# Kernel optimization log

Hardware: AMD Instinct MI355X
Metric: run time of the kernel (lower is better)

## Reference

```python
import jax, jax.numpy as jnp
import numpy as np

NUME = 100000
H, DH, K, R = 4, 32, 16, 17
DIN, DT, DOUT = 128, 32, 128
N0, N1, N2 = 131072, 32768, 4096
B, HIST = 2048, 2
LN_EPS = 1e-5


def setup_inputs() -> dict:
    key = jax.random.key(0)
    ks = jax.random.split(key, 16)
    din = DIN + DT
    inp = {}
    inp["emb"] = jax.random.normal(ks[0], (NUME, DIN), jnp.float32) * 0.1
    inp["freq"] = jnp.asarray(1.0 / 10 ** np.linspace(0, 9, DT), jnp.float32)
    inp["phase"] = jnp.zeros((DT,), jnp.float32)
    for l in (0, 1):
        inp[f"gamma{l}"] = jnp.ones((din,), jnp.float32)
        inp[f"beta{l}"] = jnp.zeros((din,), jnp.float32)
        inp[f"W{l}"] = jax.random.normal(ks[1 + 5 * l], (R, din, H * DH), jnp.float32) * 0.05
        inp[f"attn_l{l}"] = jax.random.normal(ks[2 + 5 * l], (R, H, DH), jnp.float32) * 0.05
        inp[f"attn_r{l}"] = jax.random.normal(ks[3 + 5 * l], (R, H, DH), jnp.float32) * 0.05
        inp[f"bias{l}"] = jnp.zeros((R, H * DH), jnp.float32)
    inp["src_ids0"] = jax.random.randint(ks[11], (N0,), 0, NUME * 100)
    inp["src_idx0"] = jax.random.randint(ks[12], (R, N1, K), 0, N0)
    inp["src_ids1"] = jax.random.randint(ks[13], (N1,), 0, NUME * 100)
    inp["src_idx1"] = jax.random.randint(ks[14], (R, N2, K), 0, N1)
    inp["root_idx"] = jax.random.randint(ks[15], (B * HIST,), 0, N2)
    inp["ts"] = 99
    return inp


def _gat_layer(h, src_ids, src_idx, gamma, beta, W, al, ar, b, ts, freq, phase):
    # h: [Nsrc, din-DT] src-node features; src_idx: [R, Ndst, K] neighbor ids.
    ndst = src_idx.shape[1]
    # TimeEnc: cos((ts - nid // nume) * freq + phase)
    t = (ts - src_ids // NUME).astype(h.dtype)
    phi = jnp.cos(t[:, None] * freq + phase)  # [Nsrc, DT]
    h = jnp.concatenate([h, phi], axis=1)
    # LayerNorm
    mu = jnp.mean(h, axis=-1, keepdims=True)
    var = jnp.mean((h - mu) ** 2, axis=-1, keepdims=True)
    h = (h - mu) * jax.lax.rsqrt(var + LN_EPS) * gamma + beta

    def body(acc, xs):
        Wr, alr, arr, br, idx = xs
        proj = (h @ Wr).reshape(-1, H, DH)               # [Nsrc, H, DH]
        el = jnp.einsum('nhe,he->nh', proj, alr)         # [Nsrc, H]
        er = jnp.einsum('nhe,he->nh', proj[:ndst], arr)  # [Ndst, H]
        e = jax.nn.leaky_relu(el[idx] + er[:, None, :], 0.2)  # [Ndst, K, H]
        a = jax.nn.softmax(e, axis=1)                    # edge softmax over K
        out = jnp.einsum('ikh,ikhe->ihe', a, proj[idx]) + br.reshape(H, DH)
        return acc + out, None

    acc, _ = jax.lax.scan(body, jnp.zeros((ndst, H, DH), h.dtype),
                          (W, al, ar, b, src_idx))
    # HeteroGraphConv aggregate='mean' over R relation outputs, then ReLU
    return jax.nn.relu((acc / R).reshape(ndst, H * DH))


def reference(emb, freq, phase,
              gamma0, beta0, W0, attn_l0, attn_r0, bias0,
              gamma1, beta1, W1, attn_l1, attn_r1, bias1,
              src_ids0, src_idx0, src_ids1, src_idx1, root_idx, ts):
    h = emb[src_ids0 % NUME]  # entity embedding lookup [N0, DIN]
    h = _gat_layer(h, src_ids0, src_idx0, gamma0, beta0, W0, attn_l0, attn_r0,
                   bias0, ts, freq, phase)
    h = _gat_layer(h, src_ids1, src_idx1, gamma1, beta1, W1, attn_l1, attn_r1,
                   bias1, ts, freq, phase)
    # gather root embeddings and fold hist dimension into features
    return h[root_idx].reshape(B, HIST * DOUT)
```

## Files before the change

kernel.cpp:

```cpp
#include <hip/hip_runtime.h>
#include <hip/hip_bf16.h>

#define NUME 100000
constexpr int H      = 4;
constexpr int DH     = 32;
constexpr int KNB    = 16;
constexpr int R      = 17;
constexpr int DIN    = 128;
constexpr int DT     = 32;
constexpr int DINT   = 160;
constexpr int N0     = 131072;
constexpr int N1     = 32768;
constexpr int N2     = 4096;
constexpr float LN_EPS = 1e-5f;

typedef unsigned short ushort_t;
typedef ushort_t us4 __attribute__((ext_vector_type(4)));
typedef ushort_t us8 __attribute__((ext_vector_type(8)));
typedef short    s8v __attribute__((ext_vector_type(8)));
typedef float    f32x4 __attribute__((ext_vector_type(4)));

__device__ __forceinline__ float bf2f(ushort_t u) {
    return __uint_as_float(((unsigned int)u) << 16);
}
__device__ __forceinline__ ushort_t f2bf(float f) {
    unsigned int x = __float_as_uint(f);
    unsigned int r = x + 0x7fffu + ((x >> 16) & 1u);
    return (ushort_t)(r >> 16);
}

__global__ __launch_bounds__(256) void k_wcast(
    const float* __restrict__ W, ushort_t* __restrict__ wt, int total)
{
    int t = blockIdx.x * blockDim.x + threadIdx.x;
    if (t >= total) return;
    int r   = t / (DINT * DIN);
    int rem = t % (DINT * DIN);
    int k   = rem >> 7;
    int n   = rem & 127;
    wt[(size_t)r * DIN * DINT + (size_t)n * DINT + k] = f2bf(W[t]);
}

__global__ __launch_bounds__(256) void k_bsum(
    const float* __restrict__ b0, const float* __restrict__ b1,
    float* __restrict__ bsum01)
{
    int t = threadIdx.x;
    const float* b = (t < 128) ? b0 : b1;
    int c = t & 127;
    float s = 0.f;
    #pragma unroll
    for (int r = 0; r < R; ++r) s += b[r * 128 + c];
    bsum01[t] = s;
}

__global__ __launch_bounds__(256) void k_prep(
    const float* __restrict__ srcf,
    const int*   __restrict__ ids,
    const int*   __restrict__ ts_ptr,
    const float* __restrict__ freq,
    const float* __restrict__ phase,
    const float* __restrict__ gamma,
    const float* __restrict__ beta,
    const float* __restrict__ bsum,
    ushort_t*    __restrict__ hn,
    int n_rows, int mode)
{
    int wv   = (int)((blockIdx.x * blockDim.x + threadIdx.x) >> 6);
    int lane = threadIdx.x & 63;
    int half = lane >> 5;
    int l5   = lane & 31;
    int row  = wv * 2 + half;
    if (row >= n_rows) return;

    int id = ids[row];
    const float* rp = (mode == 1)
        ? (srcf + (size_t)(id % NUME) * DIN)
        : (srcf + (size_t)row * DIN);

    float4 x = *(const float4*)&rp[l5 * 4];
    if (mode == 0) {
        const float4 bs = *(const float4*)&bsum[l5 * 4];
        x.x = fmaxf((x.x + bs.x) * (1.f / (float)R), 0.f);
        x.y = fmaxf((x.y + bs.y) * (1.f / (float)R), 0.f);
        x.z = fmaxf((x.z + bs.z) * (1.f / (float)R), 0.f);
        x.w = fmaxf((x.w + bs.w) * (1.f / (float)R), 0.f);
    }

    int   ts = ts_ptr[0];
    float t  = (float)(ts - id / NUME);
    float p  = cosf(t * freq[l5] + phase[l5]);

    float s  = x.x + x.y + x.z + x.w + p;
    float sq = x.x*x.x + x.y*x.y + x.z*x.z + x.w*x.w + p*p;
    #pragma unroll
    for (int m = 1; m < 32; m <<= 1) {
        s  += __shfl_xor(s,  m);
        sq += __shfl_xor(sq, m);
    }
    float mu   = s / (float)DINT;
    float var  = sq / (float)DINT - mu * mu;
    float rstd = rsqrtf(var + LN_EPS);

    size_t base = (size_t)row * DINT;
    us4 pk;
    pk[0] = f2bf((x.x - mu) * rstd * gamma[l5*4+0] + beta[l5*4+0]);
    pk[1] = f2bf((x.y - mu) * rstd * gamma[l5*4+1] + beta[l5*4+1]);
    pk[2] = f2bf((x.z - mu) * rstd * gamma[l5*4+2] + beta[l5*4+2]);
    pk[3] = f2bf((x.w - mu) * rstd * gamma[l5*4+3] + beta[l5*4+3]);
    *(us4*)&hn[base + l5*4] = pk;
    hn[base + 128 + l5] = f2bf((p - mu) * rstd * gamma[128 + l5] + beta[128 + l5]);
}

__global__ __launch_bounds__(256) void k_gemm(
    const ushort_t* __restrict__ A,
    const ushort_t* __restrict__ BtB,
    const float*    __restrict__ alB,
    const float*    __restrict__ arB,
    ushort_t*       __restrict__ CB,
    float*          __restrict__ elB,
    float*          __restrict__ erB,
    int ndst, int M)
{
    __shared__ ushort_t Bs[128][168];
    __shared__ ushort_t As[2][128][40];

    int r = blockIdx.y;
    const ushort_t* Bt = BtB + (size_t)r * DIN * DINT;
    const float*    al = alB + (size_t)r * DIN;
    const float*    ar = arB + (size_t)r * DIN;
    ushort_t*       C  = CB  + (size_t)r * M * DIN;
    float*          el = elB + (size_t)r * M * 4;
    float*          er = erB + (size_t)r * ndst * 4;

    int tid  = threadIdx.x;
    int lane = tid & 63;
    int wave = tid >> 6;
    int wr   = wave >> 1;
    int wc   = wave & 1;
    int row0 = blockIdx.x * 128;

    {
        int bm  = tid >> 1;
        int bko = (tid & 1) * 80;
        #pragma unroll
        for (int g = 0; g < 10; ++g)
            *(us8*)&Bs[bm][bko + g * 8] =
                *(const us8*)&Bt[(size_t)bm * DINT + bko + g * 8];
        #pragma unroll
        for (int j = 0; j < 2; ++j) {
            int f  = tid + j * 256;
            int m  = f >> 2;
            int ko = (f & 3) * 8;
            *(us8*)&As[0][m][ko] = *(const us8*)&A[(size_t)(row0 + m) * DINT + ko];
        }
    }
    __syncthreads();

    s8v breg[5][4];
    #pragma unroll
    for (int kk = 0; kk < 5; ++kk)
        #pragma unroll
        for (int j = 0; j < 4; ++j)
            breg[kk][j] = *(const s8v*)&Bs[wc*64 + j*16 + (lane & 15)]
                                          [kk*32 + (lane >> 4) * 8];

    f32x4 acc[4][4];
    #pragma unroll
    for (int i = 0; i < 4; ++i)
        #pragma unroll
        for (int j = 0; j < 4; ++j) acc[i][j] = (f32x4){0.f, 0.f, 0.f, 0.f};

    #pragma unroll
    for (int kc = 0; kc < 5; ++kc) {
        us8 pa[2];
        int m0 = 0, ko0 = 0, m1 = 0, ko1 = 0;
        if (kc < 4) {
            int f0 = tid;
            m0  = f0 >> 2; ko0 = (f0 & 3) * 8;
            pa[0] = *(const us8*)&A[(size_t)(row0 + m0) * DINT + (kc + 1) * 32 + ko0];
            int f1 = tid + 256;
            m1  = f1 >> 2; ko1 = (f1 & 3) * 8;
            pa[1] = *(const us8*)&A[(size_t)(row0 + m1) * DINT + (kc + 1) * 32 + ko1];
        }

        s8v af[4];
        #pragma unroll
        for (int i = 0; i < 4; ++i)
            af[i] = *(const s8v*)&As[kc & 1][wr*64 + i*16 + (lane & 15)]
                                            [(lane >> 4) * 8];
        #pragma unroll
        for (int i = 0; i < 4; ++i)
            #pragma unroll
            for (int j = 0; j < 4; ++j)
                acc[i][j] = __builtin_amdgcn_mfma_f32_16x16x32_bf16(
                                af[i], breg[kc][j], acc[i][j], 0, 0, 0);

        if (kc < 4) {
            *(us8*)&As[(kc + 1) & 1][m0][ko0] = pa[0];
            *(us8*)&As[(kc + 1) & 1][m1][ko1] = pa[1];
        }
        __syncthreads();
    }

    #pragma unroll
    for (int i = 0; i < 4; ++i) {
        #pragma unroll
        for (int j = 0; j < 4; ++j) {
            int col  = wc*64 + j*16 + (lane & 15);
            int rowb = row0 + wr*64 + i*16 + ((lane >> 4) << 2);
            #pragma unroll
            for (int q = 0; q < 4; ++q)
                C[(size_t)(rowb + q) * DIN + col] = f2bf(acc[i][j][q]);
        }
    }

    float alv[4], arv[4];
    #pragma unroll
    for (int j = 0; j < 4; ++j) {
        int c = wc*64 + j*16 + (lane & 15);
        alv[j] = al[c];
        arv[j] = ar[c];
    }
    int b0 = lane & 1;
    int b1 = (lane >> 1) & 1;
    #pragma unroll
    for (int i = 0; i < 4; ++i) {
        #pragma unroll
        for (int q = 0; q < 4; ++q) {
            float pl0 = acc[i][0][q]*alv[0] + acc[i][1][q]*alv[1];
            float pl1 = acc[i][2][q]*alv[2] + acc[i][3][q]*alv[3];
            float pr0 = acc[i][0][q]*arv[0] + acc[i][1][q]*arv[1];
            float pr1 = acc[i][2][q]*arv[2] + acc[i][3][q]*arv[3];
            float t;
            t = __shfl_xor(b0 ? pl0 : pl1, 1);
            float vA = (b0 ? pl1 : pl0) + t;
            t = __shfl_xor(b0 ? pr0 : pr1, 1);
            float vB = (b0 ? pr1 : pr0) + t;
            t = __shfl_xor(b1 ? vA : vB, 2);
            float vC = (b1 ? vB : vA) + t;
            vC += __shfl_xor(vC, 4);
            vC += __shfl_xor(vC, 8);
            if ((lane & 12) == 0) {
                int row = row0 + wr*64 + i*16 + ((lane >> 4) << 2) + q;
                int h   = 2*wc + b0;
                if (!b1) {
                    el[(size_t)row * 4 + h] = vC;
                } else if (row < ndst) {
                    er[(size_t)row * 4 + h] = vC;
                }
            }
        }
    }
}

__global__ __launch_bounds__(256) void k_agg_r(
    const ushort_t* __restrict__ proj,
    const int*      __restrict__ idx,
    const float*    __restrict__ el,
    const float*    __restrict__ er,
    float*          __restrict__ accg,
    int ndst)
{
    int wid  = (int)((blockIdx.x * blockDim.x + threadIdx.x) >> 6);
    if (wid >= ndst) return;
    int l    = threadIdx.x & 63;
    int rsub = l >> 4;
    int fg   = l & 15;

    int jv = idx[(size_t)wid * KNB + (l & 15)];

    int j2[4];
    us8 v[4];
    #pragma unroll
    for (int kk = 0; kk < 4; ++kk) j2[kk] = __shfl(jv, 4*kk + rsub);
    #pragma unroll
    for (int kk = 0; kk < 4; ++kk)
        v[kk] = *(const us8*)&proj[(size_t)j2[kk] * DIN + fg * 8];

    int   jk = __shfl(jv, l >> 2);
    float e  = el[(size_t)jk * 4 + (l & 3)] + er[(size_t)wid * 4 + (l & 3)];
    e = e > 0.f ? e : 0.2f * e;
    float mx = e;
    #pragma unroll
    for (int m = 4; m < 64; m <<= 1) mx = fmaxf(mx, __shfl_xor(mx, m));
    float p = __expf(e - mx);
    float s = p;
    #pragma unroll
    for (int m = 4; m < 64; m <<= 1) s += __shfl_xor(s, m);
    float a = p / s;

    float vacc[8];
    #pragma unroll
    for (int t = 0; t < 8; ++t) vacc[t] = 0.f;
    #pragma unroll
    for (int kk = 0; kk < 4; ++kk) {
        float ak = __shfl(a, 16*kk + 4*rsub + (fg >> 2));
        #pragma unroll
        for (int t = 0; t < 8; ++t) vacc[t] = fmaf(ak, bf2f(v[kk][t]), vacc[t]);
    }
    #pragma unroll
    for (int t = 0; t < 8; ++t) {
        vacc[t] += __shfl_xor(vacc[t], 16);
        vacc[t] += __shfl_xor(vacc[t], 32);
    }
    if (l < 16) {
        float* ap = accg + (size_t)wid * DIN + l * 8;
        #pragma unroll
        for (int t = 0; t < 8; ++t) ap[t] += vacc[t];
    }
}

__global__ __launch_bounds__(256) void k_agg_all(
    const ushort_t* __restrict__ projB,
    const int*      __restrict__ idxB,
    const float*    __restrict__ elB,
    const float*    __restrict__ erB,
    float*          __restrict__ accg,
    int ndst, int nsrc)
{
    int wid  = (int)((blockIdx.x * blockDim.x + threadIdx.x) >> 6);
    if (wid >= ndst) return;
    int l    = threadIdx.x & 63;
    int rsub = l >> 4;
    int fg   = l & 15;

    float vacc[8];
    #pragma unroll
    for (int t = 0; t < 8; ++t) vacc[t] = 0.f;

    for (int r = 0; r < R; ++r) {
        const ushort_t* proj = projB + (size_t)r * nsrc * DIN;
        const int*      idx  = idxB  + (size_t)r * ndst * KNB;
        const float*    el   = elB   + (size_t)r * nsrc * 4;
        const float*    er   = erB   + (size_t)r * ndst * 4;

        int jv = idx[(size_t)wid * KNB + (l & 15)];

        int j2[4];
        us8 v[4];
        #pragma unroll
        for (int kk = 0; kk < 4; ++kk) j2[kk] = __shfl(jv, 4*kk + rsub);
        #pragma unroll
        for (int kk = 0; kk < 4; ++kk)
            v[kk] = *(const us8*)&proj[(size_t)j2[kk] * DIN + fg * 8];

        int   jk = __shfl(jv, l >> 2);
        float e  = el[(size_t)jk * 4 + (l & 3)] + er[(size_t)wid * 4 + (l & 3)];
        e = e > 0.f ? e : 0.2f * e;
        float mx = e;
        #pragma unroll
        for (int m = 4; m < 64; m <<= 1) mx = fmaxf(mx, __shfl_xor(mx, m));
        float p = __expf(e - mx);
        float s = p;
        #pragma unroll
        for (int m = 4; m < 64; m <<= 1) s += __shfl_xor(s, m);
        float a = p / s;

        #pragma unroll
        for (int kk = 0; kk < 4; ++kk) {
            float ak = __shfl(a, 16*kk + 4*rsub + (fg >> 2));
            #pragma unroll
            for (int t = 0; t < 8; ++t) vacc[t] = fmaf(ak, bf2f(v[kk][t]), vacc[t]);
        }
    }

    #pragma unroll
    for (int t = 0; t < 8; ++t) {
        vacc[t] += __shfl_xor(vacc[t], 16);
        vacc[t] += __shfl_xor(vacc[t], 32);
    }
    if (l < 16) {
        float* ap = accg + (size_t)wid * DIN + l * 8;
        #pragma unroll
        for (int t = 0; t < 8; ++t) ap[t] = vacc[t];
    }
}

__global__ __launch_bounds__(256) void k_root(
    const float* __restrict__ acc, const int* __restrict__ root,
    const float* __restrict__ bsum1, float* __restrict__ out, int n)
{
    int t = blockIdx.x * blockDim.x + threadIdx.x;
    if (t < n) {
        float x = acc[(size_t)root[t >> 7] * DIN + (t & 127)] + bsum1[t & 127];
        out[t] = fmaxf(x * (1.f / (float)R), 0.f);
    }
}

extern "C" void kernel_launch(void* const* d_in, const int* in_sizes, int n_in,
                              void* d_out, int out_size, void* d_ws, size_t ws_size,
                              hipStream_t stream)
{
    const float* emb    = (const float*)d_in[0];
    const float* freq   = (const float*)d_in[1];
    const float* phase  = (const float*)d_in[2];
    const float* gamma0 = (const float*)d_in[3];
    const float* beta0  = (const float*)d_in[4];
    const float* W0     = (const float*)d_in[5];
    const float* al0    = (const float*)d_in[6];
    const float* ar0    = (const float*)d_in[7];
    const float* b0     = (const float*)d_in[8];
    const float* gamma1 = (const float*)d_in[9];
    const float* beta1  = (const float*)d_in[10];
    const float* W1     = (const float*)d_in[11];
    const float* al1    = (const float*)d_in[12];
    const float* ar1    = (const float*)d_in[13];
    const float* b1     = (const float*)d_in[14];
    const int* src_ids0 = (const int*)d_in[15];
    const int* src_idx0 = (const int*)d_in[16];
    const int* src_ids1 = (const int*)d_in[17];
    const int* src_idx1 = (const int*)d_in[18];
    const int* root     = (const int*)d_in[19];
    const int* ts       = (const int*)d_in[20];
    float* out = (float*)d_out;

    char* cur = (char*)d_ws;
    auto carve = [&](size_t bytes) {
        char* p = cur;
        cur += (bytes + 255) & ~(size_t)255;
        return (void*)p;
    };
    ushort_t* hn    = (ushort_t*)carve((size_t)N0 * DINT * 2);
    float*    acc   = (float*)carve((size_t)N1 * DIN * 4);
    ushort_t* wt0   = (ushort_t*)carve((size_t)R * DIN * DINT * 2);
    ushort_t* wt1   = (ushort_t*)carve((size_t)R * DIN * DINT * 2);
    float*    bsum  = (float*)carve(256 * 4);
    ushort_t* proj  = (ushort_t*)carve((size_t)N0 * DIN * 2);
    float*    el0   = (float*)carve((size_t)N0 * 4 * 4);
    float*    er0   = (float*)carve((size_t)N1 * 4 * 4);
    size_t baseC = (size_t)(cur - (char*)d_ws);
    ushort_t* proj1 = (ushort_t*)carve((size_t)R * N1 * DIN * 2);
    float*    el1   = (float*)carve((size_t)R * N1 * 4 * 4);
    float*    er1   = (float*)carve((size_t)R * N2 * 4 * 4);
    size_t needB = (size_t)(cur - (char*)d_ws);
    const bool batchedL1 = (ws_size >= needB);
    (void)baseC;

    const int WTOT = R * DINT * DIN;

    k_bsum<<<1, 256, 0, stream>>>(b0, b1, bsum);
    k_wcast<<<(WTOT + 255) / 256, 256, 0, stream>>>(W0, wt0, WTOT);
    k_wcast<<<(WTOT + 255) / 256, 256, 0, stream>>>(W1, wt1, WTOT);

    hipMemsetAsync(acc, 0, (size_t)N1 * DIN * sizeof(float), stream);
    k_prep<<<N0 / 8, 256, 0, stream>>>(emb, src_ids0, ts, freq, phase,
                                       gamma0, beta0, bsum, hn, N0, 1);
    for (int r = 0; r < R; ++r) {
        k_gemm<<<dim3(N0 / 128, 1), 256, 0, stream>>>(
            hn, wt0 + (size_t)r * DIN * DINT, al0 + r * 128, ar0 + r * 128,
            proj, el0, er0, N1, N0);
        k_agg_r<<<N1 / 4, 256, 0, stream>>>(
            proj, src_idx0 + (size_t)r * N1 * KNB, el0, er0, acc, N1);
    }

    k_prep<<<N1 / 8, 256, 0, stream>>>(acc, src_ids1, ts, freq, phase,
                                       gamma1, beta1, bsum, hn, N1, 0);
    if (batchedL1) {
        k_gemm<<<dim3(N1 / 128, R), 256, 0, stream>>>(
            hn, wt1, al1, ar1, proj1, el1, er1, N2, N1);
        k_agg_all<<<N2 / 4, 256, 0, stream>>>(
            proj1, src_idx1, el1, er1, acc, N2, N1);
    } else {
        hipMemsetAsync(acc, 0, (size_t)N2 * DIN * sizeof(float), stream);
        for (int r = 0; r < R; ++r) {
            k_gemm<<<dim3(N1 / 128, 1), 256, 0, stream>>>(
                hn, wt1 + (size_t)r * DIN * DINT, al1 + r * 128, ar1 + r * 128,
                proj, el0, er0, N2, N1);
            k_agg_r<<<N2 / 4, 256, 0, stream>>>(
                proj, src_idx1 + (size_t)r * N2 * KNB, el0, er0, acc, N2);
        }
    }

    k_root<<<(N2 * DIN) / 256, 256, 0, stream>>>(acc, root, bsum + 128, out, N2 * DIN);
}
```

Measured before the change: 1.208 ms.

## Batch GAT relations in groups of four and pad LDS tiles

Relations are now processed in groups of up to four. Each group gets one batched GEMM launch and one aggregation launch that sums the group's relations in registers before a single read-modify-write of the accumulator. The first group writes the accumulator directly, so the memset is no longer needed. This cuts per-relation launches and global accumulator traffic in layer 0, and replaces the fully batched layer-1 path with the same grouped scheme to bound workspace size. The GEMM shared-memory tiles also get an odd padding (170 and 42 elements) with split 8-byte LDS accesses to reduce bank conflicts, at the cost of more LDS instructions and 8-byte accesses that may not be 8-byte aligned.

```diff
diff --git a/kernel.cpp b/kernel.cpp
--- a/kernel.cpp
+++ b/kernel.cpp
@@ -28,6 +28,18 @@
     unsigned int r = x + 0x7fffu + ((x >> 16) & 1u);
     return (ushort_t)(r >> 16);
 }
+__device__ __forceinline__ void st_us8_2(ushort_t* p, us8 v) {
+    *(us4*)p       = __builtin_shufflevector(v, v, 0, 1, 2, 3);
+    *(us4*)(p + 4) = __builtin_shufflevector(v, v, 4, 5, 6, 7);
+}
+__device__ __forceinline__ s8v ld_s8v_2(const ushort_t* p) {
+    us4 a = *(const us4*)p;
+    us4 b = *(const us4*)(p + 4);
+    us8 t = __builtin_shufflevector(a, b, 0, 1, 2, 3, 4, 5, 6, 7);
+    s8v r;
+    __builtin_memcpy(&r, &t, 16);
+    return r;
+}
 
 __global__ __launch_bounds__(256) void k_wcast(
     const float* __restrict__ W, ushort_t* __restrict__ wt, int total)
@@ -122,8 +134,8 @@
     float*          __restrict__ erB,
     int ndst, int M)
 {
-    __shared__ ushort_t Bs[128][168];
-    __shared__ ushort_t As[2][128][40];
+    __shared__ ushort_t Bs[128][170];
+    __shared__ ushort_t As[2][128][42];
 
     int r = blockIdx.y;
     const ushort_t* Bt = BtB + (size_t)r * DIN * DINT;
@@ -144,15 +156,17 @@
         int bm  = tid >> 1;
         int bko = (tid & 1) * 80;
         #pragma unroll
-        for (int g = 0; g < 10; ++g)
-            *(us8*)&Bs[bm][bko + g * 8] =
-                *(const us8*)&Bt[(size_t)bm * DINT + bko + g * 8];
+        for (int g = 0; g < 10; ++g) {
+            us8 t = *(const us8*)&Bt[(size_t)bm * DINT + bko + g * 8];
+            st_us8_2(&Bs[bm][bko + g * 8], t);
+        }
         #pragma unroll
         for (int j = 0; j < 2; ++j) {
             int f  = tid + j * 256;
             int m  = f >> 2;
             int ko = (f & 3) * 8;
-            *(us8*)&As[0][m][ko] = *(const us8*)&A[(size_t)(row0 + m) * DINT + ko];
+            us8 t = *(const us8*)&A[(size_t)(row0 + m) * DINT + ko];
+            st_us8_2(&As[0][m][ko], t);
         }
     }
     __syncthreads();
@@ -162,8 +176,8 @@
     for (int kk = 0; kk < 5; ++kk)
         #pragma unroll
         for (int j = 0; j < 4; ++j)
-            breg[kk][j] = *(const s8v*)&Bs[wc*64 + j*16 + (lane & 15)]
-                                          [kk*32 + (lane >> 4) * 8];
+            breg[kk][j] = ld_s8v_2(&Bs[wc*64 + j*16 + (lane & 15)]
+                                      [kk*32 + (lane >> 4) * 8]);
 
     f32x4 acc[4][4];
     #pragma unroll
@@ -187,8 +201,8 @@
         s8v af[4];
         #pragma unroll
         for (int i = 0; i < 4; ++i)
-            af[i] = *(const s8v*)&As[kc & 1][wr*64 + i*16 + (lane & 15)]
-                                            [(lane >> 4) * 8];
+            af[i] = ld_s8v_2(&As[kc & 1][wr*64 + i*16 + (lane & 15)]
+                                        [(lane >> 4) * 8]);
         #pragma unroll
         for (int i = 0; i < 4; ++i)
             #pragma unroll
@@ -197,8 +211,8 @@
                                 af[i], breg[kc][j], acc[i][j], 0, 0, 0);
 
         if (kc < 4) {
-            *(us8*)&As[(kc + 1) & 1][m0][ko0] = pa[0];
-            *(us8*)&As[(kc + 1) & 1][m1][ko1] = pa[1];
+            st_us8_2(&As[(kc + 1) & 1][m0][ko0], pa[0]);
+            st_us8_2(&As[(kc + 1) & 1][m1][ko1], pa[1]);
         }
         __syncthreads();
     }
@@ -254,13 +268,13 @@
     }
 }
 
-__global__ __launch_bounds__(256) void k_agg_r(
-    const ushort_t* __restrict__ proj,
-    const int*      __restrict__ idx,
-    const float*    __restrict__ el,
-    const float*    __restrict__ er,
+__global__ __launch_bounds__(256) void k_agg_grp(
+    const ushort_t* __restrict__ projB,
+    const int*      __restrict__ idxB,
+    const float*    __restrict__ elB,
+    const float*    __restrict__ erB,
     float*          __restrict__ accg,
-    int ndst)
+    int ndst, int nsrc, int gsz, int init)
 {
     int wid  = (int)((blockIdx.x * blockDim.x + threadIdx.x) >> 6);
     if (wid >= ndst) return;
@@ -268,73 +282,16 @@
     int rsub = l >> 4;
     int fg   = l & 15;
 
-    int jv = idx[(size_t)wid * KNB + (l & 15)];
-
-    int j2[4];
-    us8 v[4];
-    #pragma unroll
-    for (int kk = 0; kk < 4; ++kk) j2[kk] = __shfl(jv, 4*kk + rsub);
-    #pragma unroll
-    for (int kk = 0; kk < 4; ++kk)
-        v[kk] = *(const us8*)&proj[(size_t)j2[kk] * DIN + fg * 8];
-
-    int   jk = __shfl(jv, l >> 2);
-    float e  = el[(size_t)jk * 4 + (l & 3)] + er[(size_t)wid * 4 + (l & 3)];
-    e = e > 0.f ? e : 0.2f * e;
-    float mx = e;
-    #pragma unroll
-    for (int m = 4; m < 64; m <<= 1) mx = fmaxf(mx, __shfl_xor(mx, m));
-    float p = __expf(e - mx);
-    float s = p;
-    #pragma unroll
-    for (int m = 4; m < 64; m <<= 1) s += __shfl_xor(s, m);
-    float a = p / s;
+    const ushort_t* proj = projB;
+    const int*      idx  = idxB;
+    const float*    el   = elB;
+    const float*    er   = erB;
 
     float vacc[8];
     #pragma unroll
     for (int t = 0; t < 8; ++t) vacc[t] = 0.f;
-    #pragma unroll
-    for (int kk = 0; kk < 4; ++kk) {
-        float ak = __shfl(a, 16*kk + 4*rsub + (fg >> 2));
-        #pragma unroll
-        for (int t = 0; t < 8; ++t) vacc[t] = fmaf(ak, bf2f(v[kk][t]), vacc[t]);
-    }
-    #pragma unroll
-    for (int t = 0; t < 8; ++t) {
-        vacc[t] += __shfl_xor(vacc[t], 16);
-        vacc[t] += __shfl_xor(vacc[t], 32);
-    }
-    if (l < 16) {
-        float* ap = accg + (size_t)wid * DIN + l * 8;
-        #pragma unroll
-        for (int t = 0; t < 8; ++t) ap[t] += vacc[t];
-    }
-}
-
-__global__ __launch_bounds__(256) void k_agg_all(
-    const ushort_t* __restrict__ projB,
-    const int*      __restrict__ idxB,
-    const float*    __restrict__ elB,
-    const float*    __restrict__ erB,
-    float*          __restrict__ accg,
-    int ndst, int nsrc)
-{
-    int wid  = (int)((blockIdx.x * blockDim.x + threadIdx.x) >> 6);
-    if (wid >= ndst) return;
-    int l    = threadIdx.x & 63;
-    int rsub = l >> 4;
-    int fg   = l & 15;
-
-    float vacc[8];
-    #pragma unroll
-    for (int t = 0; t < 8; ++t) vacc[t] = 0.f;
-
-    for (int r = 0; r < R; ++r) {
-        const ushort_t* proj = projB + (size_t)r * nsrc * DIN;
-        const int*      idx  = idxB  + (size_t)r * ndst * KNB;
-        const float*    el   = elB   + (size_t)r * nsrc * 4;
-        const float*    er   = erB   + (size_t)r * ndst * 4;
-
+
+    for (int gr = 0; gr < gsz; ++gr) {
         int jv = idx[(size_t)wid * KNB + (l & 15)];
 
         int j2[4];
@@ -363,6 +320,11 @@
             #pragma unroll
             for (int t = 0; t < 8; ++t) vacc[t] = fmaf(ak, bf2f(v[kk][t]), vacc[t]);
         }
+
+        proj += (size_t)nsrc * DIN;
+        idx  += (size_t)ndst * KNB;
+        el   += (size_t)nsrc * 4;
+        er   += (size_t)ndst * 4;
     }
 
     #pragma unroll
@@ -372,8 +334,13 @@
     }
     if (l < 16) {
         float* ap = accg + (size_t)wid * DIN + l * 8;
-        #pragma unroll
-        for (int t = 0; t < 8; ++t) ap[t] = vacc[t];
+        if (init) {
+            #pragma unroll
+            for (int t = 0; t < 8; ++t) ap[t] = vacc[t];
+        } else {
+            #pragma unroll
+            for (int t = 0; t < 8; ++t) ap[t] += vacc[t];
+        }
     }
 }
 
@@ -426,50 +393,39 @@
     ushort_t* wt0   = (ushort_t*)carve((size_t)R * DIN * DINT * 2);
     ushort_t* wt1   = (ushort_t*)carve((size_t)R * DIN * DINT * 2);
     float*    bsum  = (float*)carve(256 * 4);
-    ushort_t* proj  = (ushort_t*)carve((size_t)N0 * DIN * 2);
-    float*    el0   = (float*)carve((size_t)N0 * 4 * 4);
-    float*    er0   = (float*)carve((size_t)N1 * 4 * 4);
-    size_t baseC = (size_t)(cur - (char*)d_ws);
-    ushort_t* proj1 = (ushort_t*)carve((size_t)R * N1 * DIN * 2);
-    float*    el1   = (float*)carve((size_t)R * N1 * 4 * 4);
-    float*    er1   = (float*)carve((size_t)R * N2 * 4 * 4);
-    size_t needB = (size_t)(cur - (char*)d_ws);
-    const bool batchedL1 = (ws_size >= needB);
-    (void)baseC;
+    ushort_t* projg = (ushort_t*)carve((size_t)4 * N0 * DIN * 2);
+    float*    elg   = (float*)carve((size_t)4 * N0 * 4 * 4);
+    float*    erg   = (float*)carve((size_t)4 * N1 * 4 * 4);
 
     const int WTOT = R * DINT * DIN;
+    const int gstart[6] = {0, 4, 8, 12, 16, 17};
 
     k_bsum<<<1, 256, 0, stream>>>(b0, b1, bsum);
     k_wcast<<<(WTOT + 255) / 256, 256, 0, stream>>>(W0, wt0, WTOT);
     k_wcast<<<(WTOT + 255) / 256, 256, 0, stream>>>(W1, wt1, WTOT);
 
-    hipMemsetAsync(acc, 0, (size_t)N1 * DIN * sizeof(float), stream);
     k_prep<<<N0 / 8, 256, 0, stream>>>(emb, src_ids0, ts, freq, phase,
                                        gamma0, beta0, bsum, hn, N0, 1);
-    for (int r = 0; r < R; ++r) {
-        k_gemm<<<dim3(N0 / 128, 1), 256, 0, stream>>>(
-            hn, wt0 + (size_t)r * DIN * DINT, al0 + r * 128, ar0 + r * 128,
-            proj, el0, er0, N1, N0);
-        k_agg_r<<<N1 / 4, 256, 0, stream>>>(
-            proj, src_idx0 + (size_t)r * N1 * KNB, el0, er0, acc, N1);
+    for (int g = 0; g < 5; ++g) {
+        int g0 = gstart[g], gsz = gstart[g + 1] - g0;
+        k_gemm<<<dim3(N0 / 128, gsz), 256, 0, stream>>>(
+            hn, wt0 + (size_t)g0 * DIN * DINT, al0 + g0 * 128, ar0 + g0 * 128,
+            projg, elg, erg, N1, N0);
+        k_agg_grp<<<N1 / 4, 256, 0, stream>>>(
+            projg, src_idx0 + (size_t)g0 * N1 * KNB, elg, erg,
+            acc, N1, N0, gsz, g == 0);
     }
 
     k_prep<<<N1 / 8, 256, 0, stream>>>(acc, src_ids1, ts, freq, phase,
                                        gamma1, beta1, bsum, hn, N1, 0);
-    if (batchedL1) {
-        k_gemm<<<dim3(N1 / 128, R), 256, 0, stream>>>(
-            hn, wt1, al1, ar1, proj1, el1, er1, N2, N1);
-        k_agg_all<<<N2 / 4, 256, 0, stream>>>(
-            proj1, src_idx1, el1, er1, acc, N2, N1);
-    } else {
-        hipMemsetAsync(acc, 0, (size_t)N2 * DIN * sizeof(float), stream);
-        for (int r = 0; r < R; ++r) {
-            k_gemm<<<dim3(N1 / 128, 1), 256, 0, stream>>>(
-                hn, wt1 + (size_t)r * DIN * DINT, al1 + r * 128, ar1 + r * 128,
-                proj, el0, er0, N2, N1);
-            k_agg_r<<<N2 / 4, 256, 0, stream>>>(
-                proj, src_idx1 + (size_t)r * N2 * KNB, el0, er0, acc, N2);
-        }
+    for (int g = 0; g < 5; ++g) {
+        int g0 = gstart[g], gsz = gstart[g + 1] - g0;
+        k_gemm<<<dim3(N1 / 128, gsz), 256, 0, stream>>>(
+            hn, wt1 + (size_t)g0 * DIN * DINT, al1 + g0 * 128, ar1 + g0 * 128,
+            projg, elg, erg, N2, N1);
+        k_agg_grp<<<N2 / 4, 256, 0, stream>>>(
+            projg, src_idx1 + (size_t)g0 * N2 * KNB, elg, erg,
+            acc, N2, N1, gsz, g == 0);
     }
 
     k_root<<<(N2 * DIN) / 256, 256, 0, stream>>>(acc, root, bsum + 128, out, N2 * DIN);
```

Result: slower. 2.039 ms (+68.9%).
